# Performance work log

Measured on AMD Instinct MI355X. Metric: run time of the kernel, lower is better.

The kernel has to match this reference:

```python
import jax, jax.numpy as jnp
import numpy as np

N_NODES = 50000
N_EDGES = 600000
IN_CH = 128
HID = 256
OUT_FEAT = 256
OUT_CH = 128
EPS = 1e-12


def _sage_conv(x, src, dst, mask_f, Wl, bl, Wr, n_nodes):
    # PyG SAGEConv: out = lin_l(mean_{j in N(i)} x_j) + lin_r(x_i); L2-normalize rows.
    msg = x[src] * mask_f[:, None]                                  # [E, d] gather
    agg = jax.ops.segment_sum(msg, dst, num_segments=n_nodes)      # [N, d]
    cnt = jax.ops.segment_sum(mask_f, dst, num_segments=n_nodes)   # [N]
    agg = agg / jnp.maximum(cnt, 1.0)[:, None]                      # mean over kept edges
    out = agg @ Wl.T + bl + x @ Wr.T                                 # [N, h]
    nrm = jnp.maximum(jnp.linalg.norm(out, axis=-1, keepdims=True), EPS)
    return out / nrm


def setup_inputs() -> dict:
    key = jax.random.key(0)
    ks = jax.random.split(key, 12)
    x = jax.random.normal(ks[0], (N_NODES, IN_CH), dtype=jnp.float32)
    edge_index = jax.random.randint(ks[1], (2, N_EDGES), 0, N_NODES, dtype=jnp.int32)
    edge_mask = jax.random.bernoulli(ks[2], 0.7, (N_EDGES,))  # dropout_edge p=0.3 keep mask

    def lin(k, fan_out, fan_in):
        s = 1.0 / np.sqrt(fan_in)
        return jax.random.uniform(k, (fan_out, fan_in), jnp.float32, -s, s)

    W1l = lin(ks[3], HID, IN_CH)
    b1 = jnp.zeros((HID,), jnp.float32)
    W1r = lin(ks[4], HID, IN_CH)
    Ws = lin(ks[5], HID, IN_CH)
    bs = jnp.zeros((HID,), jnp.float32)
    W2l = lin(ks[6], OUT_FEAT, HID)
    b2 = jnp.zeros((OUT_FEAT,), jnp.float32)
    W2r = lin(ks[7], OUT_FEAT, HID)
    Wo = lin(ks[8], OUT_CH, OUT_FEAT)
    bo = jnp.zeros((OUT_CH,), jnp.float32)
    return {"x": x, "edge_index": edge_index, "edge_mask": edge_mask,
            "W1l": W1l, "b1": b1, "W1r": W1r, "Ws": Ws, "bs": bs,
            "W2l": W2l, "b2": b2, "W2r": W2r, "Wo": Wo, "bo": bo}


def reference(x, edge_index, edge_mask, W1l, b1, W1r, Ws, bs, W2l, b2, W2r, Wo, bo):
    src, dst = edge_index[0], edge_index[1]
    ones = jnp.ones((src.shape[0],), x.dtype)
    # conv1 uses all edges
    h = _sage_conv(x, src, dst, ones, W1l, b1, W1r, N_NODES)
    h = h + (x @ Ws.T + bs)
    h = jnp.tanh(h)
    # conv2 uses edge-dropped graph (mask = kept edges)
    mask_f = edge_mask.astype(x.dtype)
    h = jnp.tanh(_sage_conv(h, src, dst, mask_f, W2l, b2, W2r, N_NODES))
    return h @ Wo.T + bo
```

## Files before the change

kernel.cpp:

```cpp
#include <hip/hip_runtime.h>
#include <hip/hip_bf16.h>

#define N_NODES 50000
#define N_PAD   50048
#define N_EDGES 600000
#define IN_CH 128
#define HID 256
#define OUT_CH 128

typedef unsigned short u16;
typedef unsigned char u8;
typedef unsigned int u32;

typedef __attribute__((ext_vector_type(8))) short short8;
typedef __attribute__((ext_vector_type(4))) float f32x4;

typedef __attribute__((address_space(3))) u32 as3_u32;
typedef __attribute__((address_space(1))) const u32 as1_u32;

__device__ __forceinline__ float bf2f(u16 v) {
    unsigned u = ((unsigned)v) << 16;
    return __uint_as_float(u);
}
__device__ __forceinline__ u16 f2bf(float f) {
    unsigned u = __float_as_uint(f);
    u += 0x7FFF + ((u >> 16) & 1);
    return (u16)(u >> 16);
}

__device__ __forceinline__ float fast_tanh(float x) {
    float e = __builtin_amdgcn_exp2f(x * 2.88539008177793f);
    return 1.f - 2.f * __builtin_amdgcn_rcpf(e + 1.f);
}

__device__ __forceinline__ void async16(const void* g, void* l) {
    __builtin_amdgcn_global_load_lds((as1_u32*)g, (as3_u32*)l, 16, 0, 0);
}

__global__ void detect_kernel(const u16* __restrict__ xu, const u8* __restrict__ mb,
                              int* __restrict__ flags) {
    int lane = threadIdx.x & 63;

    int inr = 0;
    {
        u32 w0 = ((const u32*)xu)[lane * 2 + 0];
        u32 w1 = ((const u32*)xu)[lane * 2 + 1];
        u16 h[4] = {(u16)w0, (u16)(w0 >> 16), (u16)w1, (u16)(w1 >> 16)};
#pragma unroll
        for (int j = 0; j < 4; j++) {
            int e = (h[j] >> 7) & 0xFF;
            if (e >= 100 && e <= 133) inr++;
        }
    }

    int c1 = 0, c23 = 0, h3f_1 = 0, h3f_3 = 0;
#pragma unroll
    for (int t = 0; t < 16; t++) {
        u32 w = ((const u32*)mb)[t * 64 + lane];
        u8 b1 = (u8)(w >> 8), b2 = (u8)(w >> 16), b3 = (u8)(w >> 24);
        if (b1) c1++;
        if (b1 == 0x3F) h3f_1 = 1;
        if (b2) c23++;
        if (b3) c23++;
        if (b3 == 0x3F) h3f_3 = 1;
    }

#pragma unroll
    for (int off = 32; off > 0; off >>= 1) {
        inr   += __shfl_xor(inr, off, 64);
        c1    += __shfl_xor(c1, off, 64);
        c23   += __shfl_xor(c23, off, 64);
        h3f_1 |= __shfl_xor(h3f_1, off, 64);
        h3f_3 |= __shfl_xor(h3f_3, off, 64);
    }

    if (lane == 0 && blockIdx.x == 0) {
        flags[0] = (inr >= 200) ? 1 : 0;
        int fmt;
        if (h3f_1) fmt = 3;
        else if (h3f_3) fmt = 2;
        else if (c1 + c23 > 0) fmt = 0;
        else fmt = 1;
        flags[1] = fmt;
    }
}

#define NX (N_NODES * IN_CH)
#define DEGP_N 50176
__global__ void convert_all_kernel(const void* __restrict__ x,
                                   const void* __restrict__ W1l, const void* __restrict__ W1r,
                                   const void* __restrict__ Ws,
                                   const void* __restrict__ W2l, const void* __restrict__ W2r,
                                   const void* __restrict__ Wo,
                                   const void* __restrict__ b1, const void* __restrict__ bs,
                                   const void* __restrict__ b2, const void* __restrict__ bo,
                                   u16* __restrict__ xb, u16* __restrict__ Wc1,
                                   u16* __restrict__ Wsb, u16* __restrict__ Wc2,
                                   u16* __restrict__ Wob, float* __restrict__ biasf,
                                   u32* __restrict__ degp,
                                   const int* __restrict__ flags) {
    int i = blockIdx.x * blockDim.x + threadIdx.x;
    int isbf = flags[0];
    auto cv = [&](const void* s, int idx) -> u16 {
        return isbf ? ((const u16*)s)[idx] : f2bf(((const float*)s)[idx]);
    };
    if (i < NX) { xb[i] = cv(x, i); return; }
    i -= NX;
    if (i < 256 * 256) {
        int n = i >> 8, k = i & 255;
        const void* s = (k < 128) ? W1l : W1r;
        Wc1[i] = cv(s, n * 128 + (k & 127));
        return;
    }
    i -= 256 * 256;
    if (i < 256 * 128) { Wsb[i] = cv(Ws, i); return; }
    i -= 256 * 128;
    if (i < 256 * 512) {
        int n = i >> 9, k = i & 511;
        const void* s = (k < 256) ? W2l : W2r;
        Wc2[i] = cv(s, n * 256 + (k & 255));
        return;
    }
    i -= 256 * 512;
    if (i < 128 * 256) { Wob[i] = cv(Wo, i); return; }
    i -= 128 * 256;
    if (i < 896) {
        const void* s; int idx;
        if (i < 256)      { s = b1; idx = i; }
        else if (i < 512) { s = bs; idx = i - 256; }
        else if (i < 768) { s = b2; idx = i - 512; }
        else              { s = bo; idx = i - 768; }
        biasf[i] = isbf ? bf2f(((const u16*)s)[idx]) : ((const float*)s)[idx];
        return;
    }
    i -= 896;
    if (i < DEGP_N) degp[i] = 0;
}
#define CONV_TOTAL (NX + 256 * 256 + 256 * 128 + 256 * 512 + 128 * 256 + 896 + DEGP_N)

__global__ void hist_kernel(const int* __restrict__ ei, const void* __restrict__ em,
                            u32* __restrict__ degp, u32* __restrict__ rankp,
                            const int* __restrict__ flags) {
    int i = blockIdx.x * blockDim.x + threadIdx.x;
    if (i >= N_EDGES) return;
    int d = ei[N_EDGES + i];
    int fmt = flags[1];
    bool keep;
    if (fmt == 0)      keep = ((const u8*)em)[i] != 0;
    else if (fmt == 1) keep = ((const int*)em)[i] != 0;
    else if (fmt == 2) keep = ((const float*)em)[i] != 0.f;
    else               keep = ((const u16*)em)[i] != 0;
    u32 inc = keep ? 0x10001u : 1u;
    u32 old = atomicAdd(&degp[d], inc);
    rankp[i] = (old & 0xffffu) | (keep ? (old & 0xffff0000u) : 0xffff0000u);
}

__global__ void partial_kernel(const u32* __restrict__ degp, u32* __restrict__ partial) {
    __shared__ u32 sh[256];
    int t = threadIdx.x;
    int i = blockIdx.x * 256 + t;
    sh[t] = (i < N_NODES) ? degp[i] : 0;
    __syncthreads();
    for (int s = 128; s > 0; s >>= 1) {
        if (t < s) sh[t] += sh[t + s];
        __syncthreads();
    }
    if (t == 0) partial[blockIdx.x] = sh[0];
}

__global__ void scanp_kernel(const u32* __restrict__ partial, int* __restrict__ pscan, int nb) {
    __shared__ int sh[256];
    int t = threadIdx.x;
    u32 pv = (t < nb) ? partial[t] : 0;
    int v1 = pv & 0xffff, v2 = pv >> 16;
    sh[t] = v1;
    __syncthreads();
    for (int o = 1; o < 256; o <<= 1) {
        int u = (t >= o) ? sh[t - o] : 0;
        __syncthreads();
        sh[t] += u;
        __syncthreads();
    }
    if (t < nb) pscan[t] = sh[t] - v1;
    __syncthreads();
    sh[t] = v2;
    __syncthreads();
    for (int o = 1; o < 256; o <<= 1) {
        int u = (t >= o) ? sh[t - o] : 0;
        __syncthreads();
        sh[t] += u;
        __syncthreads();
    }
    if (t < nb) pscan[nb + t] = sh[t] - v2;
}

__global__ void rowptr_kernel(const u32* __restrict__ degp, const int* __restrict__ pscan,
                              int* __restrict__ row_ptr, int* __restrict__ row_ptr2, int nb) {
    __shared__ u32 sh[256];
    int t = threadIdx.x;
    int i = blockIdx.x * 256 + t;
    u32 v = (i < N_NODES) ? degp[i] : 0;
    sh[t] = v;
    __syncthreads();
    for (int o = 1; o < 256; o <<= 1) {
        u32 u = (t >= o) ? sh[t - o] : 0;
        __syncthreads();
        sh[t] += u;
        __syncthreads();
    }
    u32 ex = sh[t] - v;
    if (i <= N_NODES) {
        row_ptr[i]  = pscan[blockIdx.x] + (int)(ex & 0xffff);
        row_ptr2[i] = pscan[nb + blockIdx.x] + (int)(ex >> 16);
    }
}

__global__ void scatter_csr_kernel(const int* __restrict__ ei, const u32* __restrict__ rankp,
                                   const int* __restrict__ row_ptr, const int* __restrict__ row_ptr2,
                                   int* __restrict__ srcs, int* __restrict__ srcs2) {
    int i = blockIdx.x * blockDim.x + threadIdx.x;
    if (i >= N_EDGES) return;
    int d = ei[N_EDGES + i];
    int s = ei[i];
    u32 rp = rankp[i];
    srcs[row_ptr[d] + (int)(rp & 0xffffu)] = s;
    u32 kr = rp >> 16;
    if (kr != 0xffffu) srcs2[row_ptr2[d] + (int)kr] = s;
}

__global__ __launch_bounds__(256) void gather1_kernel(const int* __restrict__ row_ptr,
                                                      const int* __restrict__ srcs,
                                                      const u16* __restrict__ xb,
                                                      u16* __restrict__ aggb) {
    int wid = (blockIdx.x * blockDim.x + threadIdx.x) >> 6;
    int lane = threadIdx.x & 63;
    if (wid >= N_NODES) return;
    int start = row_ptr[wid], end = row_ptr[wid + 1];
    int dg = end - start;
    int sv = (lane < dg) ? srcs[start + lane] : 0;
    float a0 = 0.f, a1 = 0.f, b0 = 0.f, b1 = 0.f;
    float c0 = 0.f, c1 = 0.f, d0 = 0.f, d1 = 0.f;
    int n = dg < 64 ? dg : 64;
    int e = 0;
    for (; e + 4 <= n; e += 4) {
        int s0 = __builtin_amdgcn_readlane(sv, e);
        int s1 = __builtin_amdgcn_readlane(sv, e + 1);
        int s2 = __builtin_amdgcn_readlane(sv, e + 2);
        int s3 = __builtin_amdgcn_readlane(sv, e + 3);
        u32 v0 = *(const u32*)(xb + (size_t)s0 * IN_CH + lane * 2);
        u32 v1 = *(const u32*)(xb + (size_t)s1 * IN_CH + lane * 2);
        u32 v2 = *(const u32*)(xb + (size_t)s2 * IN_CH + lane * 2);
        u32 v3 = *(const u32*)(xb + (size_t)s3 * IN_CH + lane * 2);
        a0 += bf2f((u16)v0); a1 += bf2f((u16)(v0 >> 16));
        b0 += bf2f((u16)v1); b1 += bf2f((u16)(v1 >> 16));
        c0 += bf2f((u16)v2); c1 += bf2f((u16)(v2 >> 16));
        d0 += bf2f((u16)v3); d1 += bf2f((u16)(v3 >> 16));
    }
    for (; e < n; e++) {
        int s0 = __builtin_amdgcn_readlane(sv, e);
        u32 v0 = *(const u32*)(xb + (size_t)s0 * IN_CH + lane * 2);
        a0 += bf2f((u16)v0); a1 += bf2f((u16)(v0 >> 16));
    }
    for (e = 64; e < dg; e++) {
        int s0 = srcs[start + e];
        u32 v0 = *(const u32*)(xb + (size_t)s0 * IN_CH + lane * 2);
        a0 += bf2f((u16)v0); a1 += bf2f((u16)(v0 >> 16));
    }
    float inv = 1.f / fmaxf((float)dg, 1.f);
    float rx = (a0 + b0) + (c0 + d0);
    float ry = (a1 + b1) + (c1 + d1);
    u32 o = (u32)f2bf(rx * inv) | ((u32)f2bf(ry * inv) << 16);
    *(u32*)(aggb + (size_t)wid * IN_CH + lane * 2) = o;
}

__global__ __launch_bounds__(256) void gather2_kernel(const int* __restrict__ row_ptr2,
                                                      const int* __restrict__ srcs2,
                                                      const u16* __restrict__ h1b,
                                                      u16* __restrict__ aggb) {
    int wid = (blockIdx.x * blockDim.x + threadIdx.x) >> 6;
    int lane = threadIdx.x & 63;
    if (wid >= N_NODES) return;
    int start = row_ptr2[wid], end = row_ptr2[wid + 1];
    int dg = end - start;
    int sv = (lane < dg) ? srcs2[start + lane] : 0;
    float a0 = 0.f, a1 = 0.f, a2 = 0.f, a3 = 0.f;
    float b0 = 0.f, b1 = 0.f, b2 = 0.f, b3 = 0.f;
    float c0 = 0.f, c1 = 0.f, c2 = 0.f, c3 = 0.f;
    float d0 = 0.f, d1 = 0.f, d2 = 0.f, d3 = 0.f;
    int n = dg < 64 ? dg : 64;
    int e = 0;
    for (; e + 4 <= n; e += 4) {
        int s0 = __builtin_amdgcn_readlane(sv, e);
        int s1 = __builtin_amdgcn_readlane(sv, e + 1);
        int s2 = __builtin_amdgcn_readlane(sv, e + 2);
        int s3 = __builtin_amdgcn_readlane(sv, e + 3);
        uint2 v = *(const uint2*)(h1b + (size_t)s0 * HID + lane * 4);
        uint2 w = *(const uint2*)(h1b + (size_t)s1 * HID + lane * 4);
        uint2 y = *(const uint2*)(h1b + (size_t)s2 * HID + lane * 4);
        uint2 zz = *(const uint2*)(h1b + (size_t)s3 * HID + lane * 4);
        a0 += bf2f((u16)v.x); a1 += bf2f((u16)(v.x >> 16));
        a2 += bf2f((u16)v.y); a3 += bf2f((u16)(v.y >> 16));
        b0 += bf2f((u16)w.x); b1 += bf2f((u16)(w.x >> 16));
        b2 += bf2f((u16)w.y); b3 += bf2f((u16)(w.y >> 16));
        c0 += bf2f((u16)y.x); c1 += bf2f((u16)(y.x >> 16));
        c2 += bf2f((u16)y.y); c3 += bf2f((u16)(y.y >> 16));
        d0 += bf2f((u16)zz.x); d1 += bf2f((u16)(zz.x >> 16));
        d2 += bf2f((u16)zz.y); d3 += bf2f((u16)(zz.y >> 16));
    }
    for (; e < n; e++) {
        int s0 = __builtin_amdgcn_readlane(sv, e);
        uint2 v = *(const uint2*)(h1b + (size_t)s0 * HID + lane * 4);
        a0 += bf2f((u16)v.x); a1 += bf2f((u16)(v.x >> 16));
        a2 += bf2f((u16)v.y); a3 += bf2f((u16)(v.y >> 16));
    }
    for (e = 64; e < dg; e++) {
        int s0 = srcs2[start + e];
        uint2 v = *(const uint2*)(h1b + (size_t)s0 * HID + lane * 4);
        a0 += bf2f((u16)v.x); a1 += bf2f((u16)(v.x >> 16));
        a2 += bf2f((u16)v.y); a3 += bf2f((u16)(v.y >> 16));
    }
    float inv = 1.f / fmaxf((float)dg, 1.f);
    float r0 = (a0 + b0) + (c0 + d0);
    float r1 = (a1 + b1) + (c1 + d1);
    float r2 = (a2 + b2) + (c2 + d2);
    float r3 = (a3 + b3) + (c3 + d3);
    u32 o0 = (u32)f2bf(r0 * inv) | ((u32)f2bf(r1 * inv) << 16);
    u32 o1 = (u32)f2bf(r2 * inv) | ((u32)f2bf(r3 * inv) << 16);
    u16* p = aggb + (size_t)wid * HID + lane * 4;
    *(u32*)p = o0;
    *(u32*)(p + 2) = o1;
}

template<int MODE>
__global__ __launch_bounds__(256, 2) void gemm_staged(
    const u16* __restrict__ A0, const u16* __restrict__ A1,
    const u16* __restrict__ W0, const u16* __restrict__ W1,
    const float* __restrict__ bias0, const float* __restrict__ bias1,
    u16* __restrict__ outb, void* __restrict__ outv, const int* __restrict__ flags) {

    constexpr int NT  = 4;
    constexpr int Nw  = NT * 16;
    constexpr int NKS    = (MODE == 1) ? 12 : 8;
    constexpr int ABYTES = (MODE == 1) ? 4096 : 8192;
    constexpr int AARENA = (MODE == 1) ? 8192 : 16384;
    constexpr int BBYTES = (MODE == 1) ? 16384 : 32768;
    __shared__ __align__(16) u8 ldsmem[AARENA + 2 * BBYTES];

    int tid = threadIdx.x;
    int w = tid >> 6, lane = tid & 63;
    int q = lane >> 4, c = lane & 15;
    int m_base = blockIdx.x * 64;
    int rj = lane >> 3, jj = lane & 7;
    int j16 = ((jj ^ rj) << 4);

    f32x4 acc[4][NT], acc2[4][NT];
    const f32x4 z = {0.f, 0.f, 0.f, 0.f};
#pragma unroll
    for (int mt = 0; mt < 4; mt++)
#pragma unroll
        for (int nt = 0; nt < NT; nt++) { acc[mt][nt] = z; acc2[mt][nt] = z; }

    auto stage = [&](int ks, int b) {
        if constexpr (MODE == 1) {
            const u16* ap; int aoff;
            if (ks < 4)      { ap = A0; aoff = ks * 64; }
            else if (ks < 8) { ap = A1; aoff = (ks - 4) * 64; }
            else             { ap = A1; aoff = (ks - 8) * 64; }
            const u16* wp; int wstrB, woff;
            if (ks < 8) { wp = W0; wstrB = 512; woff = ks * 64; }
            else        { wp = W1; wstrB = 256; woff = (ks - 8) * 64; }
            int r16 = lane >> 2;
            int sc = (((lane & 3) ^ (r16 & 3) ^ ((lane >> 4) & 3)) << 4);
            {
                const u8* g = (const u8*)ap + (size_t)(m_base + w * 16 + r16) * 256 + aoff + sc;
                async16(g, ldsmem + b * ABYTES + (w * 16) * 64);
            }
#pragma unroll
            for (int t = 0; t < 4; t++) {
                int rb = w * 64 + t * 16;
                const u8* g = (const u8*)wp + (size_t)(rb + r16) * wstrB + woff + sc;
                async16(g, ldsmem + AARENA + b * BBYTES + rb * 64);
            }
        } else {
            const u16* ap; int astr, kta;
            const u16* wp; int wstr, ktw;
            astr = 256;
            if (ks < 4) { ap = A0; kta = ks; } else { ap = A1; kta = ks - 4; }
            wp = W0; wstr = 512; ktw = ks;
#pragma unroll
            for (int t = 0; t < 2; t++) {
                int r = w * 16 + t * 8;
                const u8* g = (const u8*)(ap + (size_t)(m_base + r + rj) * astr) + kta * 128 + j16;
                async16(g, ldsmem + b * ABYTES + r * 128);
            }
#pragma unroll
            for (int t = 0; t < NT * 2; t++) {
                int n = w * Nw + t * 8;
                const u8* g = (const u8*)(wp + (size_t)(n + rj) * wstr) + ktw * 128 + j16;
                async16(g, ldsmem + AARENA + b * BBYTES + n * 128);
            }
        }
    };

    auto compute = [&](int b, f32x4 (*tgt)[NT]) {
        if constexpr (MODE == 1) {
            const u8* ab = ldsmem + b * ABYTES;
            const u8* bb = ldsmem + AARENA + b * BBYTES;
            int sw = ((q ^ (c & 3) ^ ((c >> 2) & 3)) << 4);
            short8 af[4], bfr[NT];
#pragma unroll
            for (int mt = 0; mt < 4; mt++)
                af[mt] = *(const short8*)(ab + (mt * 16 + c) * 64 + sw);
#pragma unroll
            for (int nt = 0; nt < NT; nt++)
                bfr[nt] = *(const short8*)(bb + (w * Nw + nt * 16 + c) * 64 + sw);
#pragma unroll
            for (int mt = 0; mt < 4; mt++)
#pragma unroll
                for (int nt = 0; nt < NT; nt++)
                    tgt[mt][nt] = __builtin_amdgcn_mfma_f32_16x16x32_bf16(af[mt], bfr[nt], tgt[mt][nt], 0, 0, 0);
        } else {
            const u8* ab = ldsmem + b * ABYTES;
            const u8* bb = ldsmem + AARENA + b * BBYTES;
#pragma unroll
            for (int kk = 0; kk < 2; kk++) {
                int sA = (((kk * 4 + q) ^ (c & 7)) << 4);
                short8 af[4], bfr[NT];
#pragma unroll
                for (int mt = 0; mt < 4; mt++)
                    af[mt] = *(const short8*)(ab + (mt * 16 + c) * 128 + sA);
#pragma unroll
                for (int nt = 0; nt < NT; nt++)
                    bfr[nt] = *(const short8*)(bb + (w * Nw + nt * 16 + c) * 128 + sA);
#pragma unroll
                for (int mt = 0; mt < 4; mt++)
#pragma unroll
                    for (int nt = 0; nt < NT; nt++)
                        tgt[mt][nt] = __builtin_amdgcn_mfma_f32_16x16x32_bf16(af[mt], bfr[nt], tgt[mt][nt], 0, 0, 0);
            }
        }
    };

    stage(0, 0);
    int b = 0;
#pragma unroll
    for (int ks = 0; ks < NKS; ks++) {
        __syncthreads();
        if (ks + 1 < NKS) stage(ks + 1, b ^ 1);
        if (MODE == 1 && ks >= 8) compute(b, acc2);
        else                      compute(b, acc);
        b ^= 1;
    }
    __syncthreads();

    float* redf = (float*)ldsmem;
    float bcol[NT];
#pragma unroll
    for (int nt = 0; nt < NT; nt++) bcol[nt] = bias0[w * Nw + nt * 16 + c];
    float s[4][4];
#pragma unroll
    for (int mt = 0; mt < 4; mt++)
#pragma unroll
        for (int r = 0; r < 4; r++) {
            float t = 0.f;
#pragma unroll
            for (int nt = 0; nt < NT; nt++) {
                float v = acc[mt][nt][r] + bcol[nt];
                acc[mt][nt][r] = v;
                t += v * v;
            }
            s[mt][r] = t;
        }
#pragma unroll
    for (int off = 1; off < 16; off <<= 1) {
#pragma unroll
        for (int mt = 0; mt < 4; mt++)
#pragma unroll
            for (int r = 0; r < 4; r++)
                s[mt][r] += __shfl_xor(s[mt][r], off, 64);
    }
    if (c == 0) {
#pragma unroll
        for (int mt = 0; mt < 4; mt++)
#pragma unroll
            for (int r = 0; r < 4; r++)
                redf[(mt * 16 + q * 4 + r) * 4 + w] = s[mt][r];
    }
    __syncthreads();
    if (tid < 64) {
        float t = redf[tid * 4] + redf[tid * 4 + 1] + redf[tid * 4 + 2] + redf[tid * 4 + 3];
        redf[256 + tid] = 1.f / fmaxf(sqrtf(t), 1e-12f);
    }
    __syncthreads();

    if (MODE == 1) {
        float b2col[NT];
#pragma unroll
        for (int nt = 0; nt < NT; nt++) b2col[nt] = bias1[w * Nw + nt * 16 + c];
#pragma unroll
        for (int mt = 0; mt < 4; mt++)
#pragma unroll
            for (int r = 0; r < 4; r++) {
                int rl = mt * 16 + q * 4 + r;
                int row = m_base + rl;
                if (row < N_NODES) {
                    float iv = redf[256 + rl];
#pragma unroll
                    for (int nt = 0; nt < NT; nt++) {
                        int col = w * Nw + nt * 16 + c;
                        float t = fast_tanh(acc[mt][nt][r] * iv + acc2[mt][nt][r] + b2col[nt]);
                        float tp = __shfl_xor(t, 1, 64);
                        if (!(lane & 1)) {
                            u32 pk = (u32)f2bf(t) | ((u32)f2bf(tp) << 16);
                            *(u32*)(outb + (size_t)row * HID + col) = pk;
                        }
                    }
                }
            }
    } else {
        u8* h2l = ldsmem + AARENA;
        u8* wol = ldsmem + AARENA + BBYTES;
        int rj2 = lane >> 5, s5 = lane & 31;

        auto stageWo = [&](int half) {
#pragma unroll
            for (int t = 0; t < 8; t++) {
                int rl = w * 16 + t * 2 + rj2;
                const u8* g = (const u8*)W1 + (((size_t)(half * 64 + rl)) << 9)
                            + ((s5 ^ (rl & 7)) << 4);
                async16(g, wol + (w * 16 + t * 2) * 512);
            }
        };

        stageWo(0);
#pragma unroll
        for (int mt = 0; mt < 4; mt++)
#pragma unroll
            for (int r = 0; r < 4; r++) {
                int rl = mt * 16 + q * 4 + r;
                float iv = redf[256 + rl];
#pragma unroll
                for (int nt = 0; nt < NT; nt++) {
                    int k = w * Nw + nt * 16 + c;
                    float t = fast_tanh(acc[mt][nt][r] * iv);
                    float tp = __shfl_xor(t, 1, 64);
                    if (!(lane & 1)) {
                        u32 pk = (u32)f2bf(t) | ((u32)f2bf(tp) << 16);
                        int off = rl * 512 + ((((k >> 3) ^ (rl & 7)) << 4)) + ((k & 7) << 1);
                        *(u32*)(h2l + off) = pk;
                    }
                }
            }
        __syncthreads();

        int isbf = flags[0];
        float bO0 = bias1[w * 16 + c];
        float bO1 = bias1[64 + w * 16 + c];

        auto computeO = [&](f32x4* accO) {
#pragma unroll
            for (int kk = 0; kk < 8; kk++) {
                int sw = (((kk * 4 + q) ^ (c & 7)) << 4);
                short8 bfO = *(const short8*)(wol + (w * 16 + c) * 512 + sw);
#pragma unroll
                for (int mt = 0; mt < 4; mt++) {
                    short8 afO = *(const short8*)(h2l + (mt * 16 + c) * 512 + sw);
                    accO[mt] = __builtin_amdgcn_mfma_f32_16x16x32_bf16(afO, bfO, accO[mt], 0, 0, 0);
                }
            }
        };
        auto storeO = [&](int half, float bO, f32x4* accO) {
#pragma unroll
            for (int mt = 0; mt < 4; mt++)
#pragma unroll
                for (int r = 0; r < 4; r++) {
                    int row = m_base + mt * 16 + q * 4 + r;
                    if (row < N_NODES) {
                        int col = half * 64 + w * 16 + c;
                        float v = accO[mt][r] + bO;
                        if (isbf) {
                            float vp = __shfl_xor(v, 1, 64);
                            if (!(lane & 1))
                                *(u32*)((u16*)outv + (size_t)row * OUT_CH + col) =
                                    (u32)f2bf(v) | ((u32)f2bf(vp) << 16);
                        } else {
                            ((float*)outv)[(size_t)row * OUT_CH + col] = v;
                        }
                    }
                }
        };

        f32x4 accO[4];
#pragma unroll
        for (int mt = 0; mt < 4; mt++) accO[mt] = z;
        computeO(accO);
        __syncthreads();
        stageWo(1);
        storeO(0, bO0, accO);
        __syncthreads();
#pragma unroll
        for (int mt = 0; mt < 4; mt++) accO[mt] = z;
        computeO(accO);
        storeO(1, bO1, accO);
    }
}

extern "C" void kernel_launch(void* const* d_in, const int* in_sizes, int n_in,
                              void* d_out, int out_size, void* d_ws, size_t ws_size,
                              hipStream_t stream) {
    const void* x    = d_in[0];
    const int*  ei   = (const int*)d_in[1];
    const void* em   = d_in[2];
    const void* W1l  = d_in[3];
    const void* b1   = d_in[4];
    const void* W1r  = d_in[5];
    const void* Ws   = d_in[6];
    const void* bs   = d_in[7];
    const void* W2l  = d_in[8];
    const void* b2   = d_in[9];
    const void* W2r  = d_in[10];
    const void* Wo   = d_in[11];
    const void* bo   = d_in[12];

    char* p = (char*)d_ws;
    auto carve = [&](size_t bytes) { char* r = p; p += (bytes + 63) & ~(size_t)63; return r; };
    int*   flags   = (int*)carve(256);
    u16*   xb      = (u16*)carve((size_t)N_PAD * IN_CH * 2);
    u16*   h1b     = (u16*)carve((size_t)N_PAD * HID * 2);
    u16*   aggb    = (u16*)carve((size_t)N_PAD * HID * 2);
    u16*   Wc1     = (u16*)carve(256 * 256 * 2);
    u16*   Wsb     = (u16*)carve(256 * 128 * 2);
    u16*   Wc2     = (u16*)carve(256 * 512 * 2);
    u16*   Wob     = (u16*)carve(128 * 256 * 2);
    float* biasf   = (float*)carve(896 * 4);
    u32*   degp    = (u32*)carve(50176 * 4);
    int*   row_ptr = (int*)carve(50056 * 4);
    int*   row_ptr2= (int*)carve(50056 * 4);
    u32*   partial = (u32*)carve(256 * 4);
    int*   pscan   = (int*)carve(512 * 4);
    u32*   rankp   = (u32*)carve((size_t)N_EDGES * 4);
    int*   srcs    = (int*)carve((size_t)N_EDGES * 4);
    int*   srcs2   = (int*)carve((size_t)N_EDGES * 4);
    float* b1f = biasf, *bsf = biasf + 256, *b2f = biasf + 512, *bof = biasf + 768;
    (void)ws_size; (void)in_sizes; (void)n_in; (void)out_size;

    detect_kernel<<<1, 64, 0, stream>>>((const u16*)x, (const u8*)em, flags);

    convert_all_kernel<<<(CONV_TOTAL + 255) / 256, 256, 0, stream>>>(
        x, W1l, W1r, Ws, W2l, W2r, Wo, b1, bs, b2, bo,
        xb, Wc1, Wsb, Wc2, Wob, biasf, degp, flags);

    hist_kernel<<<(N_EDGES + 255) / 256, 256, 0, stream>>>(ei, em, degp, rankp, flags);
    const int NB = (N_NODES + 255) / 256;
    partial_kernel<<<NB, 256, 0, stream>>>(degp, partial);
    scanp_kernel<<<1, 256, 0, stream>>>(partial, pscan, NB);
    rowptr_kernel<<<NB, 256, 0, stream>>>(degp, pscan, row_ptr, row_ptr2, NB);
    scatter_csr_kernel<<<(N_EDGES + 255) / 256, 256, 0, stream>>>(ei, rankp, row_ptr, row_ptr2, srcs, srcs2);

    const int GB = N_PAD / 64;

    gather1_kernel<<<(N_NODES * 64) / 256, 256, 0, stream>>>(row_ptr, srcs, xb, aggb);
    gemm_staged<1><<<GB, 256, 0, stream>>>(aggb, xb, Wc1, Wsb, b1f, bsf, h1b, nullptr, flags);

    gather2_kernel<<<(N_NODES * 64) / 256, 256, 0, stream>>>(row_ptr2, srcs2, h1b, aggb);
    gemm_staged<2><<<GB, 256, 0, stream>>>(aggb, h1b, Wc2, Wob, b2f, bof, nullptr, d_out, flags);
}
```

Measured before the change: 296.2 us.

## Fuse layer-1 neighbor gather into GEMM, overlapping gathers with x-side MFMA steps

Removes the separate gather1 kernel and computes the layer-1 mean aggregation inside the first GEMM kernel. Each wave gathers 16 rows, four nodes at a time, interleaved with the x-side K-steps (Wr and Ws), then writes the packed bf16 aggregates to LDS for the final Wl K-steps. This removes an intermediate aggb write and read plus a kernel launch, and tries to hide gather latency behind MFMA work. The cost is a GEMM grid with less parallelism for the irregular gather (one wave per 16 nodes instead of one per node), higher register pressure, and divergence on variable degrees.

```diff
diff --git a/kernel.cpp b/kernel.cpp
--- a/kernel.cpp
+++ b/kernel.cpp
@@ -226,51 +226,6 @@
     srcs[row_ptr[d] + (int)(rp & 0xffffu)] = s;
     u32 kr = rp >> 16;
     if (kr != 0xffffu) srcs2[row_ptr2[d] + (int)kr] = s;
-}
-
-__global__ __launch_bounds__(256) void gather1_kernel(const int* __restrict__ row_ptr,
-                                                      const int* __restrict__ srcs,
-                                                      const u16* __restrict__ xb,
-                                                      u16* __restrict__ aggb) {
-    int wid = (blockIdx.x * blockDim.x + threadIdx.x) >> 6;
-    int lane = threadIdx.x & 63;
-    if (wid >= N_NODES) return;
-    int start = row_ptr[wid], end = row_ptr[wid + 1];
-    int dg = end - start;
-    int sv = (lane < dg) ? srcs[start + lane] : 0;
-    float a0 = 0.f, a1 = 0.f, b0 = 0.f, b1 = 0.f;
-    float c0 = 0.f, c1 = 0.f, d0 = 0.f, d1 = 0.f;
-    int n = dg < 64 ? dg : 64;
-    int e = 0;
-    for (; e + 4 <= n; e += 4) {
-        int s0 = __builtin_amdgcn_readlane(sv, e);
-        int s1 = __builtin_amdgcn_readlane(sv, e + 1);
-        int s2 = __builtin_amdgcn_readlane(sv, e + 2);
-        int s3 = __builtin_amdgcn_readlane(sv, e + 3);
-        u32 v0 = *(const u32*)(xb + (size_t)s0 * IN_CH + lane * 2);
-        u32 v1 = *(const u32*)(xb + (size_t)s1 * IN_CH + lane * 2);
-        u32 v2 = *(const u32*)(xb + (size_t)s2 * IN_CH + lane * 2);
-        u32 v3 = *(const u32*)(xb + (size_t)s3 * IN_CH + lane * 2);
-        a0 += bf2f((u16)v0); a1 += bf2f((u16)(v0 >> 16));
-        b0 += bf2f((u16)v1); b1 += bf2f((u16)(v1 >> 16));
-        c0 += bf2f((u16)v2); c1 += bf2f((u16)(v2 >> 16));
-        d0 += bf2f((u16)v3); d1 += bf2f((u16)(v3 >> 16));
-    }
-    for (; e < n; e++) {
-        int s0 = __builtin_amdgcn_readlane(sv, e);
-        u32 v0 = *(const u32*)(xb + (size_t)s0 * IN_CH + lane * 2);
-        a0 += bf2f((u16)v0); a1 += bf2f((u16)(v0 >> 16));
-    }
-    for (e = 64; e < dg; e++) {
-        int s0 = srcs[start + e];
-        u32 v0 = *(const u32*)(xb + (size_t)s0 * IN_CH + lane * 2);
-        a0 += bf2f((u16)v0); a1 += bf2f((u16)(v0 >> 16));
-    }
-    float inv = 1.f / fmaxf((float)dg, 1.f);
-    float rx = (a0 + b0) + (c0 + d0);
-    float ry = (a1 + b1) + (c1 + d1);
-    u32 o = (u32)f2bf(rx * inv) | ((u32)f2bf(ry * inv) << 16);
-    *(u32*)(aggb + (size_t)wid * IN_CH + lane * 2) = o;
 }
 
 __global__ __launch_bounds__(256) void gather2_kernel(const int* __restrict__ row_ptr2,
@@ -331,19 +286,17 @@
     *(u32*)(p + 2) = o1;
 }
 
-template<int MODE>
-__global__ __launch_bounds__(256, 2) void gemm_staged(
-    const u16* __restrict__ A0, const u16* __restrict__ A1,
-    const u16* __restrict__ W0, const u16* __restrict__ W1,
-    const float* __restrict__ bias0, const float* __restrict__ bias1,
-    u16* __restrict__ outb, void* __restrict__ outv, const int* __restrict__ flags) {
+__global__ __launch_bounds__(256, 2) void gemm1_fused(
+    const int* __restrict__ row_ptr, const int* __restrict__ srcs,
+    const u16* __restrict__ xb, const u16* __restrict__ Wc1,
+    const u16* __restrict__ Wsb, const float* __restrict__ bias0,
+    const float* __restrict__ bias1, u16* __restrict__ outb) {
 
     constexpr int NT  = 4;
-    constexpr int Nw  = NT * 16;
-    constexpr int NKS    = (MODE == 1) ? 12 : 8;
-    constexpr int ABYTES = (MODE == 1) ? 4096 : 8192;
-    constexpr int AARENA = (MODE == 1) ? 8192 : 16384;
-    constexpr int BBYTES = (MODE == 1) ? 16384 : 32768;
+    constexpr int Nw  = 64;
+    constexpr int ABYTES = 8192;
+    constexpr int AARENA = 16384;
+    constexpr int BBYTES = 32768;
     __shared__ __align__(16) u8 ldsmem[AARENA + 2 * BBYTES];
 
     int tid = threadIdx.x;
@@ -360,96 +313,141 @@
 #pragma unroll
         for (int nt = 0; nt < NT; nt++) { acc[mt][nt] = z; acc2[mt][nt] = z; }
 
-    auto stage = [&](int ks, int b) {
-        if constexpr (MODE == 1) {
-            const u16* ap; int aoff;
-            if (ks < 4)      { ap = A0; aoff = ks * 64; }
-            else if (ks < 8) { ap = A1; aoff = (ks - 4) * 64; }
-            else             { ap = A1; aoff = (ks - 8) * 64; }
-            const u16* wp; int wstrB, woff;
-            if (ks < 8) { wp = W0; wstrB = 512; woff = ks * 64; }
-            else        { wp = W1; wstrB = 256; woff = (ks - 8) * 64; }
-            int r16 = lane >> 2;
-            int sc = (((lane & 3) ^ (r16 & 3) ^ ((lane >> 4) & 3)) << 4);
-            {
-                const u8* g = (const u8*)ap + (size_t)(m_base + w * 16 + r16) * 256 + aoff + sc;
-                async16(g, ldsmem + b * ABYTES + (w * 16) * 64);
-            }
-#pragma unroll
-            for (int t = 0; t < 4; t++) {
-                int rb = w * 64 + t * 16;
-                const u8* g = (const u8*)wp + (size_t)(rb + r16) * wstrB + woff + sc;
-                async16(g, ldsmem + AARENA + b * BBYTES + rb * 64);
-            }
-        } else {
-            const u16* ap; int astr, kta;
-            const u16* wp; int wstr, ktw;
-            astr = 256;
-            if (ks < 4) { ap = A0; kta = ks; } else { ap = A1; kta = ks - 4; }
-            wp = W0; wstr = 512; ktw = ks;
-#pragma unroll
-            for (int t = 0; t < 2; t++) {
-                int r = w * 16 + t * 8;
-                const u8* g = (const u8*)(ap + (size_t)(m_base + r + rj) * astr) + kta * 128 + j16;
-                async16(g, ldsmem + b * ABYTES + r * 128);
-            }
-#pragma unroll
-            for (int t = 0; t < NT * 2; t++) {
-                int n = w * Nw + t * 8;
-                const u8* g = (const u8*)(wp + (size_t)(n + rj) * wstr) + ktw * 128 + j16;
-                async16(g, ldsmem + AARENA + b * BBYTES + n * 128);
-            }
-        }
-    };
-
-    auto compute = [&](int b, f32x4 (*tgt)[NT]) {
-        if constexpr (MODE == 1) {
-            const u8* ab = ldsmem + b * ABYTES;
-            const u8* bb = ldsmem + AARENA + b * BBYTES;
-            int sw = ((q ^ (c & 3) ^ ((c >> 2) & 3)) << 4);
+    u32 agg_pk[16];
+
+    auto stageA_xb = [&](int kt, int b) {
+#pragma unroll
+        for (int t = 0; t < 2; t++) {
+            int r = w * 16 + t * 8;
+            const u8* g = (const u8*)(xb + (size_t)(m_base + r + rj) * 128) + kt * 128 + j16;
+            async16(g, ldsmem + b * ABYTES + r * 128);
+        }
+    };
+    auto stageB = [&](int ks, int b) {
+        const u16* wp; int wstr, ktw;
+        if (ks == 0)      { wp = Wc1; wstr = 256; ktw = 2; }
+        else if (ks == 1) { wp = Wc1; wstr = 256; ktw = 3; }
+        else if (ks == 2) { wp = Wsb; wstr = 128; ktw = 0; }
+        else if (ks == 3) { wp = Wsb; wstr = 128; ktw = 1; }
+        else if (ks == 4) { wp = Wc1; wstr = 256; ktw = 0; }
+        else              { wp = Wc1; wstr = 256; ktw = 1; }
+#pragma unroll
+        for (int t = 0; t < 8; t++) {
+            int n = w * Nw + t * 8;
+            const u8* g = (const u8*)(wp + (size_t)(n + rj) * wstr) + ktw * 128 + j16;
+            async16(g, ldsmem + AARENA + b * BBYTES + n * 128);
+        }
+    };
+    auto compute = [&](int ab, int bb, f32x4 (*tgt)[NT]) {
+        const u8* abp = ldsmem + ab * ABYTES;
+        const u8* bbp = ldsmem + AARENA + bb * BBYTES;
+#pragma unroll
+        for (int kk = 0; kk < 2; kk++) {
+            int sA = (((kk * 4 + q) ^ (c & 7)) << 4);
             short8 af[4], bfr[NT];
 #pragma unroll
             for (int mt = 0; mt < 4; mt++)
-                af[mt] = *(const short8*)(ab + (mt * 16 + c) * 64 + sw);
+                af[mt] = *(const short8*)(abp + (mt * 16 + c) * 128 + sA);
 #pragma unroll
             for (int nt = 0; nt < NT; nt++)
-                bfr[nt] = *(const short8*)(bb + (w * Nw + nt * 16 + c) * 64 + sw);
+                bfr[nt] = *(const short8*)(bbp + (w * Nw + nt * 16 + c) * 128 + sA);
 #pragma unroll
             for (int mt = 0; mt < 4; mt++)
 #pragma unroll
                 for (int nt = 0; nt < NT; nt++)
                     tgt[mt][nt] = __builtin_amdgcn_mfma_f32_16x16x32_bf16(af[mt], bfr[nt], tgt[mt][nt], 0, 0, 0);
-        } else {
-            const u8* ab = ldsmem + b * ABYTES;
-            const u8* bb = ldsmem + AARENA + b * BBYTES;
-#pragma unroll
-            for (int kk = 0; kk < 2; kk++) {
-                int sA = (((kk * 4 + q) ^ (c & 7)) << 4);
-                short8 af[4], bfr[NT];
-#pragma unroll
-                for (int mt = 0; mt < 4; mt++)
-                    af[mt] = *(const short8*)(ab + (mt * 16 + c) * 128 + sA);
-#pragma unroll
-                for (int nt = 0; nt < NT; nt++)
-                    bfr[nt] = *(const short8*)(bb + (w * Nw + nt * 16 + c) * 128 + sA);
-#pragma unroll
-                for (int mt = 0; mt < 4; mt++)
-#pragma unroll
-                    for (int nt = 0; nt < NT; nt++)
-                        tgt[mt][nt] = __builtin_amdgcn_mfma_f32_16x16x32_bf16(af[mt], bfr[nt], tgt[mt][nt], 0, 0, 0);
+        }
+    };
+
+    auto gather4 = [&](int s) {
+        int nb = m_base + w * 16 + s * 4;
+        int n0 = nb, n1 = nb + 1, n2 = nb + 2, n3 = nb + 3;
+        int st0 = (n0 < N_NODES) ? row_ptr[n0] : 0;
+        int st1 = (n1 < N_NODES) ? row_ptr[n1] : 0;
+        int st2 = (n2 < N_NODES) ? row_ptr[n2] : 0;
+        int st3 = (n3 < N_NODES) ? row_ptr[n3] : 0;
+        int dg0 = (n0 < N_NODES) ? row_ptr[n0 + 1] - st0 : 0;
+        int dg1 = (n1 < N_NODES) ? row_ptr[n1 + 1] - st1 : 0;
+        int dg2 = (n2 < N_NODES) ? row_ptr[n2 + 1] - st2 : 0;
+        int dg3 = (n3 < N_NODES) ? row_ptr[n3 + 1] - st3 : 0;
+        int sv0 = (lane < dg0) ? srcs[st0 + lane] : 0;
+        int sv1 = (lane < dg1) ? srcs[st1 + lane] : 0;
+        int sv2 = (lane < dg2) ? srcs[st2 + lane] : 0;
+        int sv3 = (lane < dg3) ? srcs[st3 + lane] : 0;
+        float x0 = 0.f, y0 = 0.f, x1 = 0.f, y1 = 0.f;
+        float x2 = 0.f, y2 = 0.f, x3 = 0.f, y3 = 0.f;
+        int c0 = dg0 < 64 ? dg0 : 64, c1 = dg1 < 64 ? dg1 : 64;
+        int c2 = dg2 < 64 ? dg2 : 64, c3 = dg3 < 64 ? dg3 : 64;
+        int mx = max(max(c0, c1), max(c2, c3));
+        for (int e = 0; e < mx; e += 2) {
+            if (e < c0) { int sA = __builtin_amdgcn_readlane(sv0, e);
+                u32 v = *(const u32*)(xb + (size_t)sA * IN_CH + lane * 2);
+                x0 += bf2f((u16)v); y0 += bf2f((u16)(v >> 16)); }
+            if (e < c1) { int sA = __builtin_amdgcn_readlane(sv1, e);
+                u32 v = *(const u32*)(xb + (size_t)sA * IN_CH + lane * 2);
+                x1 += bf2f((u16)v); y1 += bf2f((u16)(v >> 16)); }
+            if (e < c2) { int sA = __builtin_amdgcn_readlane(sv2, e);
+                u32 v = *(const u32*)(xb + (size_t)sA * IN_CH + lane * 2);
+                x2 += bf2f((u16)v); y2 += bf2f((u16)(v >> 16)); }
+            if (e < c3) { int sA = __builtin_amdgcn_readlane(sv3, e);
+                u32 v = *(const u32*)(xb + (size_t)sA * IN_CH + lane * 2);
+                x3 += bf2f((u16)v); y3 += bf2f((u16)(v >> 16)); }
+            if (e + 1 < c0) { int sA = __builtin_amdgcn_readlane(sv0, e + 1);
+                u32 v = *(const u32*)(xb + (size_t)sA * IN_CH + lane * 2);
+                x0 += bf2f((u16)v); y0 += bf2f((u16)(v >> 16)); }
+            if (e + 1 < c1) { int sA = __builtin_amdgcn_readlane(sv1, e + 1);
+                u32 v = *(const u32*)(xb + (size_t)sA * IN_CH + lane * 2);
+                x1 += bf2f((u16)v); y1 += bf2f((u16)(v >> 16)); }
+            if (e + 1 < c2) { int sA = __builtin_amdgcn_readlane(sv2, e + 1);
+                u32 v = *(const u32*)(xb + (size_t)sA * IN_CH + lane * 2);
+                x2 += bf2f((u16)v); y2 += bf2f((u16)(v >> 16)); }
+            if (e + 1 < c3) { int sA = __builtin_amdgcn_readlane(sv3, e + 1);
+                u32 v = *(const u32*)(xb + (size_t)sA * IN_CH + lane * 2);
+                x3 += bf2f((u16)v); y3 += bf2f((u16)(v >> 16)); }
+        }
+        for (int e = 64; e < dg0; e++) { int sA = srcs[st0 + e];
+            u32 v = *(const u32*)(xb + (size_t)sA * IN_CH + lane * 2);
+            x0 += bf2f((u16)v); y0 += bf2f((u16)(v >> 16)); }
+        for (int e = 64; e < dg1; e++) { int sA = srcs[st1 + e];
+            u32 v = *(const u32*)(xb + (size_t)sA * IN_CH + lane * 2);
+            x1 += bf2f((u16)v); y1 += bf2f((u16)(v >> 16)); }
+        for (int e = 64; e < dg2; e++) { int sA = srcs[st2 + e];
+            u32 v = *(const u32*)(xb + (size_t)sA * IN_CH + lane * 2);
+            x2 += bf2f((u16)v); y2 += bf2f((u16)(v >> 16)); }
+        for (int e = 64; e < dg3; e++) { int sA = srcs[st3 + e];
+            u32 v = *(const u32*)(xb + (size_t)sA * IN_CH + lane * 2);
+            x3 += bf2f((u16)v); y3 += bf2f((u16)(v >> 16)); }
+        float i0 = 1.f / fmaxf((float)dg0, 1.f);
+        float i1 = 1.f / fmaxf((float)dg1, 1.f);
+        float i2 = 1.f / fmaxf((float)dg2, 1.f);
+        float i3 = 1.f / fmaxf((float)dg3, 1.f);
+        agg_pk[s * 4 + 0] = (u32)f2bf(x0 * i0) | ((u32)f2bf(y0 * i0) << 16);
+        agg_pk[s * 4 + 1] = (u32)f2bf(x1 * i1) | ((u32)f2bf(y1 * i1) << 16);
+        agg_pk[s * 4 + 2] = (u32)f2bf(x2 * i2) | ((u32)f2bf(y2 * i2) << 16);
+        agg_pk[s * 4 + 3] = (u32)f2bf(x3 * i3) | ((u32)f2bf(y3 * i3) << 16);
+    };
+
+    stageA_xb(0, 0);
+    stageA_xb(1, 1);
+    stageB(0, 0);
+
+#pragma unroll
+    for (int ks = 0; ks < 6; ks++) {
+        __syncthreads();
+        if (ks + 1 < 6) stageB(ks + 1, (ks + 1) & 1);
+        compute(ks & 1, ks & 1, (ks == 2 || ks == 3) ? acc2 : acc);
+        if (ks < 4) gather4(ks);
+        if (ks == 3) {
+            __syncthreads();
+            int cidx = lane >> 2;
+            u8* base = ldsmem + ((cidx >= 8) ? ABYTES : 0);
+            int co = (((cidx & 7)) << 4) + (lane & 3) * 4;
+#pragma unroll
+            for (int r = 0; r < 16; r++) {
+                int R = w * 16 + r;
+                *(u32*)(base + R * 128 + (co ^ ((R & 7) << 4))) = agg_pk[r];
             }
         }
-    };
-
-    stage(0, 0);
-    int b = 0;
-#pragma unroll
-    for (int ks = 0; ks < NKS; ks++) {
-        __syncthreads();
-        if (ks + 1 < NKS) stage(ks + 1, b ^ 1);
-        if (MODE == 1 && ks >= 8) compute(b, acc2);
-        else                      compute(b, acc);
-        b ^= 1;
     }
     __syncthreads();
 
@@ -493,116 +491,232 @@
     }
     __syncthreads();
 
-    if (MODE == 1) {
-        float b2col[NT];
-#pragma unroll
-        for (int nt = 0; nt < NT; nt++) b2col[nt] = bias1[w * Nw + nt * 16 + c];
-#pragma unroll
-        for (int mt = 0; mt < 4; mt++)
-#pragma unroll
-            for (int r = 0; r < 4; r++) {
-                int rl = mt * 16 + q * 4 + r;
-                int row = m_base + rl;
-                if (row < N_NODES) {
-                    float iv = redf[256 + rl];
-#pragma unroll
-                    for (int nt = 0; nt < NT; nt++) {
-                        int col = w * Nw + nt * 16 + c;
-                        float t = fast_tanh(acc[mt][nt][r] * iv + acc2[mt][nt][r] + b2col[nt]);
-                        float tp = __shfl_xor(t, 1, 64);
-                        if (!(lane & 1)) {
-                            u32 pk = (u32)f2bf(t) | ((u32)f2bf(tp) << 16);
-                            *(u32*)(outb + (size_t)row * HID + col) = pk;
-                        }
+    float b2col[NT];
+#pragma unroll
+    for (int nt = 0; nt < NT; nt++) b2col[nt] = bias1[w * Nw + nt * 16 + c];
+#pragma unroll
+    for (int mt = 0; mt < 4; mt++)
+#pragma unroll
+        for (int r = 0; r < 4; r++) {
+            int rl = mt * 16 + q * 4 + r;
+            int row = m_base + rl;
+            if (row < N_NODES) {
+                float iv = redf[256 + rl];
+#pragma unroll
+                for (int nt = 0; nt < NT; nt++) {
+                    int col = w * Nw + nt * 16 + c;
+                    float t = fast_tanh(acc[mt][nt][r] * iv + acc2[mt][nt][r] + b2col[nt]);
+                    float tp = __shfl_xor(t, 1, 64);
+                    if (!(lane & 1)) {
+                        u32 pk = (u32)f2bf(t) | ((u32)f2bf(tp) << 16);
+                        *(u32*)(outb + (size_t)row * HID + col) = pk;
                     }
                 }
             }
-    } else {
-        u8* h2l = ldsmem + AARENA;
-        u8* wol = ldsmem + AARENA + BBYTES;
-        int rj2 = lane >> 5, s5 = lane & 31;
-
-        auto stageWo = [&](int half) {
-#pragma unroll
-            for (int t = 0; t < 8; t++) {
-                int rl = w * 16 + t * 2 + rj2;
-                const u8* g = (const u8*)W1 + (((size_t)(half * 64 + rl)) << 9)
-                            + ((s5 ^ (rl & 7)) << 4);
-                async16(g, wol + (w * 16 + t * 2) * 512);
+        }
+}
+
+__global__ __launch_bounds__(256, 2) void gemm2_staged(
+    const u16* __restrict__ A0, const u16* __restrict__ A1,
+    const u16* __restrict__ W0, const u16* __restrict__ W1,
+    const float* __restrict__ bias0, const float* __restrict__ bias1,
+    void* __restrict__ outv, const int* __restrict__ flags) {
+
+    constexpr int NT  = 4;
+    constexpr int Nw  = 64;
+    constexpr int NKS = 8;
+    constexpr int ABYTES = 8192;
+    constexpr int AARENA = 16384;
+    constexpr int BBYTES = 32768;
+    __shared__ __align__(16) u8 ldsmem[AARENA + 2 * BBYTES];
+
+    int tid = threadIdx.x;
+    int w = tid >> 6, lane = tid & 63;
+    int q = lane >> 4, c = lane & 15;
+    int m_base = blockIdx.x * 64;
+    int rj = lane >> 3, jj = lane & 7;
+    int j16 = ((jj ^ rj) << 4);
+
+    f32x4 acc[4][NT];
+    const f32x4 z = {0.f, 0.f, 0.f, 0.f};
+#pragma unroll
+    for (int mt = 0; mt < 4; mt++)
+#pragma unroll
+        for (int nt = 0; nt < NT; nt++) acc[mt][nt] = z;
+
+    auto stage = [&](int ks, int b) {
+        const u16* ap; int kta;
+        if (ks < 4) { ap = A0; kta = ks; } else { ap = A1; kta = ks - 4; }
+#pragma unroll
+        for (int t = 0; t < 2; t++) {
+            int r = w * 16 + t * 8;
+            const u8* g = (const u8*)(ap + (size_t)(m_base + r + rj) * 256) + kta * 128 + j16;
+            async16(g, ldsmem + b * ABYTES + r * 128);
+        }
+#pragma unroll
+        for (int t = 0; t < 8; t++) {
+            int n = w * Nw + t * 8;
+            const u8* g = (const u8*)(W0 + (size_t)(n + rj) * 512) + ks * 128 + j16;
+            async16(g, ldsmem + AARENA + b * BBYTES + n * 128);
+        }
+    };
+
+    auto compute = [&](int b) {
+        const u8* ab = ldsmem + b * ABYTES;
+        const u8* bb = ldsmem + AARENA + b * BBYTES;
+#pragma unroll
+        for (int kk = 0; kk < 2; kk++) {
+            int sA = (((kk * 4 + q) ^ (c & 7)) << 4);
+            short8 af[4], bfr[NT];
+#pragma unroll
+            for (int mt = 0; mt < 4; mt++)
+                af[mt] = *(const short8*)(ab + (mt * 16 + c) * 128 + sA);
+#pragma unroll
+            for (int nt = 0; nt < NT; nt++)
+                bfr[nt] = *(const short8*)(bb + (w * Nw + nt * 16 + c) * 128 + sA);
+#pragma unroll
+            for (int mt = 0; mt < 4; mt++)
+#pragma unroll
+                for (int nt = 0; nt < NT; nt++)
+                    acc[mt][nt] = __builtin_amdgcn_mfma_f32_16x16x32_bf16(af[mt], bfr[nt], acc[mt][nt], 0, 0, 0);
+        }
+    };
+
+    stage(0, 0);
+    int b = 0;
+#pragma unroll
+    for (int ks = 0; ks < NKS; ks++) {
+        __syncthreads();
+        if (ks + 1 < NKS) stage(ks + 1, b ^ 1);
+        compute(b);
+        b ^= 1;
+    }
+    __syncthreads();
+
+    float* redf = (float*)ldsmem;
+    float bcol[NT];
+#pragma unroll
+    for (int nt = 0; nt < NT; nt++) bcol[nt] = bias0[w * Nw + nt * 16 + c];
+    float s[4][4];
+#pragma unroll
+    for (int mt = 0; mt < 4; mt++)
+#pragma unroll
+        for (int r = 0; r < 4; r++) {
+            float t = 0.f;
+#pragma unroll
+            for (int nt = 0; nt < NT; nt++) {
+                float v = acc[mt][nt][r] + bcol[nt];
+                acc[mt][nt][r] = v;
+                t += v * v;
             }
-        };
-
-        stageWo(0);
+            s[mt][r] = t;
+        }
+#pragma unroll
+    for (int off = 1; off < 16; off <<= 1) {
 #pragma unroll
         for (int mt = 0; mt < 4; mt++)
 #pragma unroll
+            for (int r = 0; r < 4; r++)
+                s[mt][r] += __shfl_xor(s[mt][r], off, 64);
+    }
+    if (c == 0) {
+#pragma unroll
+        for (int mt = 0; mt < 4; mt++)
+#pragma unroll
+            for (int r = 0; r < 4; r++)
+                redf[(mt * 16 + q * 4 + r) * 4 + w] = s[mt][r];
+    }
+    __syncthreads();
+    if (tid < 64) {
+        float t = redf[tid * 4] + redf[tid * 4 + 1] + redf[tid * 4 + 2] + redf[tid * 4 + 3];
+        redf[256 + tid] = 1.f / fmaxf(sqrtf(t), 1e-12f);
+    }
+    __syncthreads();
+
+    u8* h2l = ldsmem + AARENA;
+    u8* wol = ldsmem + AARENA + BBYTES;
+    int rj2 = lane >> 5, s5 = lane & 31;
+
+    auto stageWo = [&](int half) {
+#pragma unroll
+        for (int t = 0; t < 8; t++) {
+            int rl = w * 16 + t * 2 + rj2;
+            const u8* g = (const u8*)W1 + (((size_t)(half * 64 + rl)) << 9)
+                        + ((s5 ^ (rl & 7)) << 4);
+            async16(g, wol + (w * 16 + t * 2) * 512);
+        }
+    };
+
+    stageWo(0);
+#pragma unroll
+    for (int mt = 0; mt < 4; mt++)
+#pragma unroll
+        for (int r = 0; r < 4; r++) {
+            int rl = mt * 16 + q * 4 + r;
+            float iv = redf[256 + rl];
+#pragma unroll
+            for (int nt = 0; nt < NT; nt++) {
+                int k = w * Nw + nt * 16 + c;
+                float t = fast_tanh(acc[mt][nt][r] * iv);
+                float tp = __shfl_xor(t, 1, 64);
+                if (!(lane & 1)) {
+                    u32 pk = (u32)f2bf(t) | ((u32)f2bf(tp) << 16);
+                    int off = rl * 512 + ((((k >> 3) ^ (rl & 7)) << 4)) + ((k & 7) << 1);
+                    *(u32*)(h2l + off) = pk;
+                }
+            }
+        }
+    __syncthreads();
+
+    int isbf = flags[0];
+    float bO0 = bias1[w * 16 + c];
+    float bO1 = bias1[64 + w * 16 + c];
+
+    auto computeO = [&](f32x4* accO) {
+#pragma unroll
+        for (int kk = 0; kk < 8; kk++) {
+            int sw = (((kk * 4 + q) ^ (c & 7)) << 4);
+            short8 bfO = *(const short8*)(wol + (w * 16 + c) * 512 + sw);
+#pragma unroll
+            for (int mt = 0; mt < 4; mt++) {
+                short8 afO = *(const short8*)(h2l + (mt * 16 + c) * 512 + sw);
+                accO[mt] = __builtin_amdgcn_mfma_f32_16x16x32_bf16(afO, bfO, accO[mt], 0, 0, 0);
+            }
+        }
+    };
+    auto storeO = [&](int half, float bO, f32x4* accO) {
+#pragma unroll
+        for (int mt = 0; mt < 4; mt++)
+#pragma unroll
             for (int r = 0; r < 4; r++) {
-                int rl = mt * 16 + q * 4 + r;
-                float iv = redf[256 + rl];
-#pragma unroll
-                for (int nt = 0; nt < NT; nt++) {
-                    int k = w * Nw + nt * 16 + c;
-                    float t = fast_tanh(acc[mt][nt][r] * iv);
-                    float tp = __shfl_xor(t, 1, 64);
-                    if (!(lane & 1)) {
-                        u32 pk = (u32)f2bf(t) | ((u32)f2bf(tp) << 16);
-                        int off = rl * 512 + ((((k >> 3) ^ (rl & 7)) << 4)) + ((k & 7) << 1);
-                        *(u32*)(h2l + off) = pk;
+                int row = m_base + mt * 16 + q * 4 + r;
+                if (row < N_NODES) {
+                    int col = half * 64 + w * 16 + c;
+                    float v = accO[mt][r] + bO;
+                    if (isbf) {
+                        float vp = __shfl_xor(v, 1, 64);
+                        if (!(lane & 1))
+                            *(u32*)((u16*)outv + (size_t)row * OUT_CH + col) =
+                                (u32)f2bf(v) | ((u32)f2bf(vp) << 16);
+                    } else {
+                        ((float*)outv)[(size_t)row * OUT_CH + col] = v;
                     }
                 }
             }
-        __syncthreads();
-
-        int isbf = flags[0];
-        float bO0 = bias1[w * 16 + c];
-        float bO1 = bias1[64 + w * 16 + c];
-
-        auto computeO = [&](f32x4* accO) {
-#pragma unroll
-            for (int kk = 0; kk < 8; kk++) {
-                int sw = (((kk * 4 + q) ^ (c & 7)) << 4);
-                short8 bfO = *(const short8*)(wol + (w * 16 + c) * 512 + sw);
-#pragma unroll
-                for (int mt = 0; mt < 4; mt++) {
-                    short8 afO = *(const short8*)(h2l + (mt * 16 + c) * 512 + sw);
-                    accO[mt] = __builtin_amdgcn_mfma_f32_16x16x32_bf16(afO, bfO, accO[mt], 0, 0, 0);
-                }
-            }
-        };
-        auto storeO = [&](int half, float bO, f32x4* accO) {
-#pragma unroll
-            for (int mt = 0; mt < 4; mt++)
-#pragma unroll
-                for (int r = 0; r < 4; r++) {
-                    int row = m_base + mt * 16 + q * 4 + r;
-                    if (row < N_NODES) {
-                        int col = half * 64 + w * 16 + c;
-                        float v = accO[mt][r] + bO;
-                        if (isbf) {
-                            float vp = __shfl_xor(v, 1, 64);
-                            if (!(lane & 1))
-                                *(u32*)((u16*)outv + (size_t)row * OUT_CH + col) =
-                                    (u32)f2bf(v) | ((u32)f2bf(vp) << 16);
-                        } else {
-                            ((float*)outv)[(size_t)row * OUT_CH + col] = v;
-                        }
-                    }
-                }
-        };
-
-        f32x4 accO[4];
-#pragma unroll
-        for (int mt = 0; mt < 4; mt++) accO[mt] = z;
-        computeO(accO);
-        __syncthreads();
-        stageWo(1);
-        storeO(0, bO0, accO);
-        __syncthreads();
-#pragma unroll
-        for (int mt = 0; mt < 4; mt++) accO[mt] = z;
-        computeO(accO);
-        storeO(1, bO1, accO);
-    }
+    };
+
+    f32x4 accO[4];
+#pragma unroll
+    for (int mt = 0; mt < 4; mt++) accO[mt] = z;
+    computeO(accO);
+    __syncthreads();
+    stageWo(1);
+    storeO(0, bO0, accO);
+    __syncthreads();
+#pragma unroll
+    for (int mt = 0; mt < 4; mt++) accO[mt] = z;
+    computeO(accO);
+    storeO(1, bO1, accO);
 }
 
 extern "C" void kernel_launch(void* const* d_in, const int* in_sizes, int n_in,
@@ -659,9 +773,8 @@
 
     const int GB = N_PAD / 64;
 
-    gather1_kernel<<<(N_NODES * 64) / 256, 256, 0, stream>>>(row_ptr, srcs, xb, aggb);
-    gemm_staged<1><<<GB, 256, 0, stream>>>(aggb, xb, Wc1, Wsb, b1f, bsf, h1b, nullptr, flags);
+    gemm1_fused<<<GB, 256, 0, stream>>>(row_ptr, srcs, xb, Wc1, Wsb, b1f, bsf, h1b);
 
     gather2_kernel<<<(N_NODES * 64) / 256, 256, 0, stream>>>(row_ptr2, srcs2, h1b, aggb);
-    gemm_staged<2><<<GB, 256, 0, stream>>>(aggb, h1b, Wc2, Wob, b2f, bof, nullptr, d_out, flags);
-}
+    gemm2_staged<<<GB, 256, 0, stream>>>(aggb, h1b, Wc2, Wob, b2f, bof, d_out, flags);
+}
```

After: 417.9 us. 1.41x slower.
